# Kernel optimization log

Hardware: AMD Instinct MI355X
Metric: run time of the kernel (lower is better)

Reference implementation:

```python
import jax, jax.numpy as jnp
import numpy as np

HIDDEN_DIM = 4096
NUM_EXPERTS = 64
TOP_K = 2
TEMPERATURE = 1.0
NUM_TOKENS = 16384


def setup_inputs() -> dict:
    key = jax.random.key(0)
    kx, kw = jax.random.split(key)
    x = jax.random.normal(kx, (NUM_TOKENS, HIDDEN_DIM), dtype=jnp.float32)
    # nn.Linear(hidden_dim, num_experts, bias=False): weight shape [num_experts, hidden_dim]
    W = jax.random.normal(kw, (NUM_EXPERTS, HIDDEN_DIM), dtype=jnp.float32) * (1.0 / np.sqrt(HIDDEN_DIM))
    return {"x": x, "W": W}


def reference(x, W):
    # gate linear: [N, H] @ [H, E] -> [N, E]
    logits = jnp.einsum("nh,eh->ne", x, W) / TEMPERATURE
    probs = jax.nn.softmax(logits, axis=-1)

    top_k_probs, top_k_indices = jax.lax.top_k(probs, TOP_K)  # [N, k]
    top_k_weights = top_k_probs / jnp.sum(top_k_probs, axis=-1, keepdims=True)

    # ---- stats (fused histogram instead of per-expert loop) ----
    expert_counts = jnp.zeros((NUM_EXPERTS,), dtype=jnp.float32).at[top_k_indices.ravel()].add(1.0)
    avg_probs = jnp.mean(probs, axis=0)
    entropy = jnp.mean(-jnp.sum(probs * jnp.log(probs + 1e-10), axis=-1))
    sorted_counts = jnp.sort(expert_counts)
    n = NUM_EXPERTS
    index = jnp.arange(1, n + 1, dtype=jnp.float32)
    gini = jnp.sum((2.0 * index - n - 1.0) * sorted_counts) / (n * jnp.sum(sorted_counts) + 1e-10)

    return (top_k_indices, top_k_weights, expert_counts, avg_probs, entropy, gini)
```

## Files before the change

### kernel.cpp

```cpp
#include <hip/hip_runtime.h>
#include <cstdint>
#include <cstddef>

#define NTOK 16384
#define HID  4096
#define NEXP 64
#define MT   128
#define KT   32
#define TPB_A 128

__device__ __forceinline__ void gload_lds16(const float* gp, float* lp) {
  __builtin_amdgcn_global_load_lds(
      (const __attribute__((address_space(1))) void*)gp,
      (__attribute__((address_space(3))) void*)lp,
      16, 0, 0);
}

__global__ __launch_bounds__(TPB_A) void gemm_part_kernel(
    const float* __restrict__ x, const float* __restrict__ W,
    float* __restrict__ part, int KS) {
  const int ntile = NTOK / MT;
  const int tile  = blockIdx.x % ntile;
  const int ks    = blockIdx.x / ntile;
  const int KRANGE = HID / KS;
  const int NKT    = KRANGE / KT;
  const int k0     = ks * KRANGE;
  const int t0     = tile * MT;

  __shared__ float xs[2][MT * KT];
  __shared__ float wsh[2][NEXP * KT];

  const int tid  = threadIdx.x;
  const int lane = tid & 63;
  const int wave = tid >> 6;
  const int tg   = tid >> 3;
  const int eg   = tid & 7;

  float acc[8][8];
#pragma unroll
  for (int i = 0; i < 8; ++i)
#pragma unroll
    for (int j = 0; j < 8; ++j) acc[i][j] = 0.f;

  auto stage = [&](int b, int kt) {
    const int kbase = k0 + kt * KT;
#pragma unroll
    for (int s = 0; s < 8; ++s) {
      int chunk = s * 2 + wave;
      int Lb  = chunk * 1024 + lane * 16;
      int row = Lb >> 7;
      int k4s = (Lb >> 4) & 7;
      int gk4 = k4s ^ (row & 7);
      const float* gp = x + (size_t)(t0 + row) * HID + kbase + gk4 * 4;
      gload_lds16(gp, &xs[b][chunk * 256]);
    }
#pragma unroll
    for (int s = 0; s < 4; ++s) {
      int chunk = s * 2 + wave;
      int Lb  = chunk * 1024 + lane * 16;
      int e   = Lb >> 7;
      int k4s = (Lb >> 4) & 7;
      int gk4 = k4s ^ ((e >> 3) & 7);
      const float* gp = W + (size_t)e * HID + kbase + gk4 * 4;
      gload_lds16(gp, &wsh[b][chunk * 256]);
    }
  };

  auto compute = [&](int b) {
    for (int k4 = 0; k4 < 8; ++k4) {
      float4 xv[8], wv[8];
#pragma unroll
      for (int i = 0; i < 8; ++i) {
        int t = tg + 16 * i;
        xv[i] = *(const float4*)&xs[b][t * 32 + ((k4 ^ (tg & 7)) << 2)];
      }
#pragma unroll
      for (int j = 0; j < 8; ++j) {
        int e = eg * 8 + j;
        wv[j] = *(const float4*)&wsh[b][e * 32 + ((k4 ^ eg) << 2)];
      }
#pragma unroll
      for (int i = 0; i < 8; ++i)
#pragma unroll
        for (int j = 0; j < 8; ++j) {
          acc[i][j] = fmaf(xv[i].x, wv[j].x, acc[i][j]);
          acc[i][j] = fmaf(xv[i].y, wv[j].y, acc[i][j]);
          acc[i][j] = fmaf(xv[i].z, wv[j].z, acc[i][j]);
          acc[i][j] = fmaf(xv[i].w, wv[j].w, acc[i][j]);
        }
    }
  };

  stage(0, 0);
  __syncthreads();
  for (int kt = 0; kt < NKT; ++kt) {
    if (kt + 1 < NKT) stage((kt + 1) & 1, kt + 1);
    compute(kt & 1);
    __syncthreads();
  }

  float* pb = part + ((size_t)ks * NTOK + t0) * NEXP;
#pragma unroll
  for (int i = 0; i < 8; ++i) {
    int t = tg + 16 * i;
    float4 o0 = make_float4(acc[i][0], acc[i][1], acc[i][2], acc[i][3]);
    float4 o1 = make_float4(acc[i][4], acc[i][5], acc[i][6], acc[i][7]);
    *(float4*)&pb[(size_t)t * NEXP + eg * 8]     = o0;
    *(float4*)&pb[(size_t)t * NEXP + eg * 8 + 4] = o1;
  }
}

__global__ __launch_bounds__(256) void router_kernel(
    const float* __restrict__ part, float* __restrict__ out,
    float* __restrict__ gstats, int KS) {
  const int lane  = threadIdx.x & 63;
  const int wave  = threadIdx.x >> 6;
  const int tbase = blockIdx.x * 64 + wave * 16;

  float avg_acc = 0.f, ent_acc = 0.f, cnt_acc = 0.f;

  for (int tt = 0; tt < 16; ++tt) {
    const int t = tbase + tt;
    float l = 0.f;
    for (int s = 0; s < KS; ++s)
      l += part[((size_t)s * NTOK + t) * NEXP + lane];

    float m = l;
#pragma unroll
    for (int off = 32; off; off >>= 1) m = fmaxf(m, __shfl_xor(m, off));
    float p = expf(l - m);
    float d = p;
#pragma unroll
    for (int off = 32; off; off >>= 1) d += __shfl_xor(d, off);
    float prob = p / d;

    avg_acc += prob;
    ent_acc += prob * logf(prob + 1e-10f);

    float v1 = prob; int i1 = lane;
#pragma unroll
    for (int off = 32; off; off >>= 1) {
      float ov = __shfl_xor(v1, off);
      int   oi = __shfl_xor(i1, off);
      if (ov > v1 || (ov == v1 && oi < i1)) { v1 = ov; i1 = oi; }
    }
    float v2 = (lane == i1) ? -1.f : prob; int i2 = lane;
#pragma unroll
    for (int off = 32; off; off >>= 1) {
      float ov = __shfl_xor(v2, off);
      int   oi = __shfl_xor(i2, off);
      if (ov > v2 || (ov == v2 && oi < i2)) { v2 = ov; i2 = oi; }
    }
    cnt_acc += (lane == i1 ? 1.f : 0.f) + (lane == i2 ? 1.f : 0.f);

    if (lane == 0) {
      float wsum = v1 + v2;
      out[2 * t]     = (float)i1;
      out[2 * t + 1] = (float)i2;
      out[2 * NTOK + 2 * t]     = v1 / wsum;
      out[2 * NTOK + 2 * t + 1] = v2 / wsum;
    }
  }

  __shared__ float red[4][NEXP];
  red[wave][lane] = avg_acc;
  __syncthreads();
  if (wave == 0) {
    float s = red[0][lane] + red[1][lane] + red[2][lane] + red[3][lane];
    atomicAdd(&gstats[NEXP + lane], s);
  }
  __syncthreads();
  red[wave][lane] = cnt_acc;
  __syncthreads();
  if (wave == 0) {
    float s = red[0][lane] + red[1][lane] + red[2][lane] + red[3][lane];
    atomicAdd(&gstats[lane], s);
  }
  float e = ent_acc;
#pragma unroll
  for (int off = 32; off; off >>= 1) e += __shfl_xor(e, off);
  __syncthreads();
  if (lane == 0) red[0][wave] = e;
  __syncthreads();
  if (threadIdx.x == 0)
    atomicAdd(&gstats[2 * NEXP], red[0][0] + red[0][1] + red[0][2] + red[0][3]);
}

__global__ void finalize_kernel(const float* __restrict__ gstats,
                                float* __restrict__ out) {
  const int e = threadIdx.x;
  const float c   = gstats[e];
  const float avg = gstats[NEXP + e] * (1.0f / NTOK);

  out[2 * NTOK * 2 + e]        = c;
  out[2 * NTOK * 2 + NEXP + e] = avg;

  __shared__ float cs[NEXP];
  cs[e] = c;
  __syncthreads();

  int rank = 0;
  for (int j = 0; j < NEXP; ++j) {
    float cj = cs[j];
    rank += (cj < c || (cj == c && j < e)) ? 1 : 0;
  }
  float val = (2.0f * (rank + 1) - NEXP - 1) * c;
  float tot = c;
#pragma unroll
  for (int off = 32; off; off >>= 1) {
    val += __shfl_xor(val, off);
    tot += __shfl_xor(tot, off);
  }
  if (e == 0) {
    out[2 * NTOK * 2 + 2 * NEXP]     = -gstats[2 * NEXP] * (1.0f / NTOK);
    out[2 * NTOK * 2 + 2 * NEXP + 1] = val / (NEXP * tot + 1e-10f);
  }
}

extern "C" void kernel_launch(void* const* d_in, const int* in_sizes, int n_in,
                              void* d_out, int out_size, void* d_ws, size_t ws_size,
                              hipStream_t stream) {
  const float* x = (const float*)d_in[0];
  const float* W = (const float*)d_in[1];
  float* out = (float*)d_out;
  float* ws  = (float*)d_ws;

  int KS;
  const size_t slab = (size_t)NTOK * NEXP * 4;
  const size_t stats_bytes = (2 * NEXP + 1) * sizeof(float);
  if      (ws_size >= 8 * slab + stats_bytes) KS = 8;
  else if (ws_size >= 4 * slab + stats_bytes) KS = 4;
  else if (ws_size >= 2 * slab + stats_bytes) KS = 2;
  else                                        KS = 1;

  float* gstats = ws + (size_t)KS * NTOK * NEXP;
  hipMemsetAsync(gstats, 0, stats_bytes, stream);

  gemm_part_kernel<<<dim3((NTOK / MT) * KS), TPB_A, 0, stream>>>(x, W, ws, KS);
  router_kernel<<<dim3(NTOK / 64), 256, 0, stream>>>(ws, out, gstats, KS);
  finalize_kernel<<<dim3(1), 64, 0, stream>>>(gstats, out);
}
```

Baseline: 503.3 us.

## Fuse gate GEMM and routing into one MFMA kernel with split-fp16 precision

Replaces the FP32 SIMT split-K GEMM plus separate router kernel with one fused kernel. It splits x and W into hi/lo fp16 pairs and uses three fp16 MFMA products to approximate fp32 accuracy, then does softmax, top-2, entropy and the stats reductions in-register with LDS atomics. This removes the partial-sum workspace round trip and the FP32 FMA compute bound. In exchange it adds per-element conversion work, direct global loads without LDS staging, and a small accuracy risk from dropping the lo*lo term.

```diff
diff --git a/kernel.cpp b/kernel.cpp
--- a/kernel.cpp
+++ b/kernel.cpp
@@ -5,185 +5,218 @@
 #define NTOK 16384
 #define HID  4096
 #define NEXP 64
-#define MT   128
-#define KT   32
-#define TPB_A 128
-
-__device__ __forceinline__ void gload_lds16(const float* gp, float* lp) {
-  __builtin_amdgcn_global_load_lds(
-      (const __attribute__((address_space(1))) void*)gp,
-      (__attribute__((address_space(3))) void*)lp,
-      16, 0, 0);
-}
-
-__global__ __launch_bounds__(TPB_A) void gemm_part_kernel(
-    const float* __restrict__ x, const float* __restrict__ W,
-    float* __restrict__ part, int KS) {
-  const int ntile = NTOK / MT;
-  const int tile  = blockIdx.x % ntile;
-  const int ks    = blockIdx.x / ntile;
-  const int KRANGE = HID / KS;
-  const int NKT    = KRANGE / KT;
-  const int k0     = ks * KRANGE;
-  const int t0     = tile * MT;
-
-  __shared__ float xs[2][MT * KT];
-  __shared__ float wsh[2][NEXP * KT];
-
-  const int tid  = threadIdx.x;
-  const int lane = tid & 63;
-  const int wave = tid >> 6;
-  const int tg   = tid >> 3;
-  const int eg   = tid & 7;
-
-  float acc[8][8];
-#pragma unroll
-  for (int i = 0; i < 8; ++i)
-#pragma unroll
-    for (int j = 0; j < 8; ++j) acc[i][j] = 0.f;
-
-  auto stage = [&](int b, int kt) {
-    const int kbase = k0 + kt * KT;
-#pragma unroll
-    for (int s = 0; s < 8; ++s) {
-      int chunk = s * 2 + wave;
-      int Lb  = chunk * 1024 + lane * 16;
-      int row = Lb >> 7;
-      int k4s = (Lb >> 4) & 7;
-      int gk4 = k4s ^ (row & 7);
-      const float* gp = x + (size_t)(t0 + row) * HID + kbase + gk4 * 4;
-      gload_lds16(gp, &xs[b][chunk * 256]);
-    }
-#pragma unroll
-    for (int s = 0; s < 4; ++s) {
-      int chunk = s * 2 + wave;
-      int Lb  = chunk * 1024 + lane * 16;
-      int e   = Lb >> 7;
-      int k4s = (Lb >> 4) & 7;
-      int gk4 = k4s ^ ((e >> 3) & 7);
-      const float* gp = W + (size_t)e * HID + kbase + gk4 * 4;
-      gload_lds16(gp, &wsh[b][chunk * 256]);
-    }
-  };
-
-  auto compute = [&](int b) {
-    for (int k4 = 0; k4 < 8; ++k4) {
-      float4 xv[8], wv[8];
-#pragma unroll
-      for (int i = 0; i < 8; ++i) {
-        int t = tg + 16 * i;
-        xv[i] = *(const float4*)&xs[b][t * 32 + ((k4 ^ (tg & 7)) << 2)];
-      }
-#pragma unroll
-      for (int j = 0; j < 8; ++j) {
-        int e = eg * 8 + j;
-        wv[j] = *(const float4*)&wsh[b][e * 32 + ((k4 ^ eg) << 2)];
-      }
-#pragma unroll
-      for (int i = 0; i < 8; ++i)
-#pragma unroll
-        for (int j = 0; j < 8; ++j) {
-          acc[i][j] = fmaf(xv[i].x, wv[j].x, acc[i][j]);
-          acc[i][j] = fmaf(xv[i].y, wv[j].y, acc[i][j]);
-          acc[i][j] = fmaf(xv[i].z, wv[j].z, acc[i][j]);
-          acc[i][j] = fmaf(xv[i].w, wv[j].w, acc[i][j]);
+#define LO_SCALE 2048.0f
+#define LO_INV   (1.0f/2048.0f)
+
+typedef _Float16 half8  __attribute__((ext_vector_type(8)));
+typedef _Float16 half4v __attribute__((ext_vector_type(4)));
+typedef float    f32x4  __attribute__((ext_vector_type(4)));
+
+__global__ __launch_bounds__(256) void wsplit_kernel(
+    const float* __restrict__ W, _Float16* __restrict__ whi,
+    _Float16* __restrict__ wlo) {
+  int i = (blockIdx.x * 256 + threadIdx.x) * 4;
+  float4 w = *(const float4*)(W + i);
+  float f[4] = {w.x, w.y, w.z, w.w};
+  half4v h, l;
+#pragma unroll
+  for (int j = 0; j < 4; ++j) {
+    float hf = __uint_as_float(__float_as_uint(f[j]) & 0xffffe000u);
+    h[j] = (_Float16)hf;
+    l[j] = (_Float16)((f[j] - hf) * LO_SCALE);
+  }
+  *(half4v*)(whi + i) = h;
+  *(half4v*)(wlo + i) = l;
+}
+
+__global__ __launch_bounds__(256, 2) void fused_kernel(
+    const float* __restrict__ x, const _Float16* __restrict__ whi,
+    const _Float16* __restrict__ wlo, float* __restrict__ out,
+    float* __restrict__ gstats) {
+  __shared__ float red[32][NEXP];
+  __shared__ float savg[NEXP];
+  __shared__ float scnt[NEXP];
+  __shared__ float sent;
+
+  const int tid     = threadIdx.x;
+  const int lane    = tid & 63;
+  const int wv      = tid >> 6;
+  const int tokhalf = wv & 1;
+  const int khalf   = wv >> 1;
+  const int row     = lane & 15;
+  const int g       = lane >> 4;
+
+  if (tid < NEXP) { savg[tid] = 0.f; scnt[tid] = 0.f; }
+  if (tid == 0) sent = 0.f;
+
+  const int t0 = blockIdx.x * 32 + tokhalf * 16;
+  const float*    xp  = x   + (size_t)(t0 + row) * HID + khalf * 2048 + g * 8;
+  const _Float16* whp = whi + (size_t)row * HID        + khalf * 2048 + g * 8;
+  const _Float16* wlp = wlo + (size_t)row * HID        + khalf * 2048 + g * 8;
+  const size_t estride = (size_t)16 * HID;
+
+  f32x4 acc[4], crs[4];
+#pragma unroll
+  for (int e = 0; e < 4; ++e) {
+    acc[e] = (f32x4){0.f, 0.f, 0.f, 0.f};
+    crs[e] = (f32x4){0.f, 0.f, 0.f, 0.f};
+  }
+
+#define LDA(KS, P0, P1)                              \
+  P0 = *(const float4*)(xp + (KS) * 32);             \
+  P1 = *(const float4*)(xp + (KS) * 32 + 4);
+
+#define LDB(KS, BH, BL)                                        \
+  _Pragma("unroll")                                            \
+  for (int e = 0; e < 4; ++e) {                                \
+    BH[e] = *(const half8*)(whp + e * estride + (KS) * 32);    \
+    BL[e] = *(const half8*)(wlp + e * estride + (KS) * 32);    \
+  }
+
+#define STEP(P0, P1, BH, BL)                                              \
+  {                                                                       \
+    float ff[8] = {P0.x, P0.y, P0.z, P0.w, P1.x, P1.y, P1.z, P1.w};       \
+    half8 ah, al;                                                         \
+    _Pragma("unroll")                                                     \
+    for (int j = 0; j < 8; ++j) {                                         \
+      float hf = __uint_as_float(__float_as_uint(ff[j]) & 0xffffe000u);   \
+      ah[j] = (_Float16)hf;                                               \
+      al[j] = (_Float16)((ff[j] - hf) * LO_SCALE);                        \
+    }                                                                     \
+    _Pragma("unroll")                                                     \
+    for (int e = 0; e < 4; ++e) {                                         \
+      acc[e] = __builtin_amdgcn_mfma_f32_16x16x32_f16(ah, BH[e], acc[e], 0, 0, 0); \
+      crs[e] = __builtin_amdgcn_mfma_f32_16x16x32_f16(ah, BL[e], crs[e], 0, 0, 0); \
+      crs[e] = __builtin_amdgcn_mfma_f32_16x16x32_f16(al, BH[e], crs[e], 0, 0, 0); \
+    }                                                                     \
+  }
+
+  float4 xa0, xa1, xb0, xb1;
+  half8 bh0[4], bl0[4], bh1[4], bl1[4];
+
+  LDA(0, xa0, xa1)
+  LDB(0, bh0, bl0)
+  for (int ks = 0; ks < 64; ks += 2) {
+    LDA(ks + 1, xb0, xb1)
+    LDB(ks + 1, bh1, bl1)
+    STEP(xa0, xa1, bh0, bl0)
+    if (ks + 2 < 64) {
+      LDA(ks + 2, xa0, xa1)
+      LDB(ks + 2, bh0, bl0)
+    }
+    STEP(xb0, xb1, bh1, bl1)
+  }
+
+  float v[4][4];
+#pragma unroll
+  for (int e = 0; e < 4; ++e)
+#pragma unroll
+    for (int r = 0; r < 4; ++r)
+      v[e][r] = acc[e][r] + crs[e][r] * LO_INV;
+
+  if (khalf == 1) {
+#pragma unroll
+    for (int e = 0; e < 4; ++e)
+#pragma unroll
+      for (int r = 0; r < 4; ++r)
+        red[tokhalf * 16 + g * 4 + r][e * 16 + row] = v[e][r];
+  }
+  __syncthreads();
+
+  if (khalf == 0) {
+#pragma unroll
+    for (int e = 0; e < 4; ++e)
+#pragma unroll
+      for (int r = 0; r < 4; ++r)
+        v[e][r] += red[tokhalf * 16 + g * 4 + r][e * 16 + row];
+
+    float m[4], S[4], PL[4];
+#pragma unroll
+    for (int r = 0; r < 4; ++r) {
+      float mm = fmaxf(fmaxf(v[0][r], v[1][r]), fmaxf(v[2][r], v[3][r]));
+#pragma unroll
+      for (int off = 1; off < 16; off <<= 1) mm = fmaxf(mm, __shfl_xor(mm, off));
+      m[r] = mm;
+    }
+    float p[4][4];
+#pragma unroll
+    for (int e = 0; e < 4; ++e)
+#pragma unroll
+      for (int r = 0; r < 4; ++r)
+        p[e][r] = __expf(v[e][r] - m[r]);
+#pragma unroll
+    for (int r = 0; r < 4; ++r) {
+      float s  = p[0][r] + p[1][r] + p[2][r] + p[3][r];
+      float pl = p[0][r] * v[0][r] + p[1][r] * v[1][r] +
+                 p[2][r] * v[2][r] + p[3][r] * v[3][r];
+#pragma unroll
+      for (int off = 1; off < 16; off <<= 1) {
+        s  += __shfl_xor(s, off);
+        pl += __shfl_xor(pl, off);
+      }
+      S[r] = s; PL[r] = pl;
+    }
+
+    float v1[4], v2[4]; int i1[4], i2[4];
+#pragma unroll
+    for (int r = 0; r < 4; ++r) {
+      float a1 = -3.4e38f, a2 = -3.4e38f; int j1 = 0, j2 = 0;
+#pragma unroll
+      for (int e = 0; e < 4; ++e) {
+        float val = v[e][r]; int idx = e * 16 + row;
+        if (val > a1)      { a2 = a1; j2 = j1; a1 = val; j1 = idx; }
+        else if (val > a2) { a2 = val; j2 = idx; }
+      }
+#pragma unroll
+      for (int off = 1; off < 16; off <<= 1) {
+        float o1 = __shfl_xor(a1, off), o2 = __shfl_xor(a2, off);
+        int  oj1 = __shfl_xor(j1, off), oj2 = __shfl_xor(j2, off);
+        if (o1 > a1 || (o1 == a1 && oj1 < j1)) {
+          if (a1 > o2 || (a1 == o2 && j1 < oj2)) { a2 = a1; j2 = j1; }
+          else                                   { a2 = o2; j2 = oj2; }
+          a1 = o1; j1 = oj1;
+        } else if (o1 > a2 || (o1 == a2 && oj1 < j2)) {
+          a2 = o1; j2 = oj1;
         }
-    }
-  };
-
-  stage(0, 0);
+      }
+      v1[r] = a1; v2[r] = a2; i1[r] = j1; i2[r] = j2;
+    }
+
+    float inv[4] = {1.f / S[0], 1.f / S[1], 1.f / S[2], 1.f / S[3]};
+
+#pragma unroll
+    for (int e = 0; e < 4; ++e) {
+      float s = p[e][0] * inv[0] + p[e][1] * inv[1] +
+                p[e][2] * inv[2] + p[e][3] * inv[3];
+      s += __shfl_xor(s, 16);
+      s += __shfl_xor(s, 32);
+      if (lane < 16) atomicAdd(&savg[e * 16 + row], s);
+    }
+
+    if (row == 0) {
+      float hsum = 0.f;
+#pragma unroll
+      for (int r = 0; r < 4; ++r) {
+        hsum += m[r] + __logf(S[r]) - PL[r] * inv[r];
+        atomicAdd(&scnt[i1[r]], 1.f);
+        atomicAdd(&scnt[i2[r]], 1.f);
+        int t = t0 + g * 4 + r;
+        float e2 = __expf(v2[r] - v1[r]);
+        float w1 = 1.f / (1.f + e2);
+        out[2 * t]     = (float)i1[r];
+        out[2 * t + 1] = (float)i2[r];
+        out[2 * NTOK + 2 * t]     = w1;
+        out[2 * NTOK + 2 * t + 1] = e2 * w1;
+      }
+      atomicAdd(&sent, hsum);
+    }
+  }
   __syncthreads();
-  for (int kt = 0; kt < NKT; ++kt) {
-    if (kt + 1 < NKT) stage((kt + 1) & 1, kt + 1);
-    compute(kt & 1);
-    __syncthreads();
-  }
-
-  float* pb = part + ((size_t)ks * NTOK + t0) * NEXP;
-#pragma unroll
-  for (int i = 0; i < 8; ++i) {
-    int t = tg + 16 * i;
-    float4 o0 = make_float4(acc[i][0], acc[i][1], acc[i][2], acc[i][3]);
-    float4 o1 = make_float4(acc[i][4], acc[i][5], acc[i][6], acc[i][7]);
-    *(float4*)&pb[(size_t)t * NEXP + eg * 8]     = o0;
-    *(float4*)&pb[(size_t)t * NEXP + eg * 8 + 4] = o1;
-  }
-}
-
-__global__ __launch_bounds__(256) void router_kernel(
-    const float* __restrict__ part, float* __restrict__ out,
-    float* __restrict__ gstats, int KS) {
-  const int lane  = threadIdx.x & 63;
-  const int wave  = threadIdx.x >> 6;
-  const int tbase = blockIdx.x * 64 + wave * 16;
-
-  float avg_acc = 0.f, ent_acc = 0.f, cnt_acc = 0.f;
-
-  for (int tt = 0; tt < 16; ++tt) {
-    const int t = tbase + tt;
-    float l = 0.f;
-    for (int s = 0; s < KS; ++s)
-      l += part[((size_t)s * NTOK + t) * NEXP + lane];
-
-    float m = l;
-#pragma unroll
-    for (int off = 32; off; off >>= 1) m = fmaxf(m, __shfl_xor(m, off));
-    float p = expf(l - m);
-    float d = p;
-#pragma unroll
-    for (int off = 32; off; off >>= 1) d += __shfl_xor(d, off);
-    float prob = p / d;
-
-    avg_acc += prob;
-    ent_acc += prob * logf(prob + 1e-10f);
-
-    float v1 = prob; int i1 = lane;
-#pragma unroll
-    for (int off = 32; off; off >>= 1) {
-      float ov = __shfl_xor(v1, off);
-      int   oi = __shfl_xor(i1, off);
-      if (ov > v1 || (ov == v1 && oi < i1)) { v1 = ov; i1 = oi; }
-    }
-    float v2 = (lane == i1) ? -1.f : prob; int i2 = lane;
-#pragma unroll
-    for (int off = 32; off; off >>= 1) {
-      float ov = __shfl_xor(v2, off);
-      int   oi = __shfl_xor(i2, off);
-      if (ov > v2 || (ov == v2 && oi < i2)) { v2 = ov; i2 = oi; }
-    }
-    cnt_acc += (lane == i1 ? 1.f : 0.f) + (lane == i2 ? 1.f : 0.f);
-
-    if (lane == 0) {
-      float wsum = v1 + v2;
-      out[2 * t]     = (float)i1;
-      out[2 * t + 1] = (float)i2;
-      out[2 * NTOK + 2 * t]     = v1 / wsum;
-      out[2 * NTOK + 2 * t + 1] = v2 / wsum;
-    }
-  }
-
-  __shared__ float red[4][NEXP];
-  red[wave][lane] = avg_acc;
-  __syncthreads();
-  if (wave == 0) {
-    float s = red[0][lane] + red[1][lane] + red[2][lane] + red[3][lane];
-    atomicAdd(&gstats[NEXP + lane], s);
-  }
-  __syncthreads();
-  red[wave][lane] = cnt_acc;
-  __syncthreads();
-  if (wave == 0) {
-    float s = red[0][lane] + red[1][lane] + red[2][lane] + red[3][lane];
-    atomicAdd(&gstats[lane], s);
-  }
-  float e = ent_acc;
-#pragma unroll
-  for (int off = 32; off; off >>= 1) e += __shfl_xor(e, off);
-  __syncthreads();
-  if (lane == 0) red[0][wave] = e;
-  __syncthreads();
-  if (threadIdx.x == 0)
-    atomicAdd(&gstats[2 * NEXP], red[0][0] + red[0][1] + red[0][2] + red[0][3]);
+  if (tid < NEXP) {
+    atomicAdd(&gstats[tid],        scnt[tid]);
+    atomicAdd(&gstats[NEXP + tid], savg[tid]);
+  }
+  if (tid == 0) atomicAdd(&gstats[2 * NEXP], sent);
 }
 
 __global__ void finalize_kernel(const float* __restrict__ gstats,
@@ -192,8 +225,8 @@
   const float c   = gstats[e];
   const float avg = gstats[NEXP + e] * (1.0f / NTOK);
 
-  out[2 * NTOK * 2 + e]        = c;
-  out[2 * NTOK * 2 + NEXP + e] = avg;
+  out[4 * NTOK + e]        = c;
+  out[4 * NTOK + NEXP + e] = avg;
 
   __shared__ float cs[NEXP];
   cs[e] = c;
@@ -212,8 +245,8 @@
     tot += __shfl_xor(tot, off);
   }
   if (e == 0) {
-    out[2 * NTOK * 2 + 2 * NEXP]     = -gstats[2 * NEXP] * (1.0f / NTOK);
-    out[2 * NTOK * 2 + 2 * NEXP + 1] = val / (NEXP * tot + 1e-10f);
+    out[4 * NTOK + 2 * NEXP]     = gstats[2 * NEXP] * (1.0f / NTOK);
+    out[4 * NTOK + 2 * NEXP + 1] = val / (NEXP * tot + 1e-10f);
   }
 }
 
@@ -223,20 +256,13 @@
   const float* x = (const float*)d_in[0];
   const float* W = (const float*)d_in[1];
   float* out = (float*)d_out;
-  float* ws  = (float*)d_ws;
-
-  int KS;
-  const size_t slab = (size_t)NTOK * NEXP * 4;
-  const size_t stats_bytes = (2 * NEXP + 1) * sizeof(float);
-  if      (ws_size >= 8 * slab + stats_bytes) KS = 8;
-  else if (ws_size >= 4 * slab + stats_bytes) KS = 4;
-  else if (ws_size >= 2 * slab + stats_bytes) KS = 2;
-  else                                        KS = 1;
-
-  float* gstats = ws + (size_t)KS * NTOK * NEXP;
-  hipMemsetAsync(gstats, 0, stats_bytes, stream);
-
-  gemm_part_kernel<<<dim3((NTOK / MT) * KS), TPB_A, 0, stream>>>(x, W, ws, KS);
-  router_kernel<<<dim3(NTOK / 64), 256, 0, stream>>>(ws, out, gstats, KS);
+
+  _Float16* whi = (_Float16*)d_ws;
+  _Float16* wlo = whi + (size_t)NEXP * HID;
+  float* gstats = (float*)(wlo + (size_t)NEXP * HID);
+
+  hipMemsetAsync(gstats, 0, (2 * NEXP + 1) * sizeof(float), stream);
+  wsplit_kernel<<<dim3((NEXP * HID) / (256 * 4)), 256, 0, stream>>>(W, whi, wlo);
+  fused_kernel<<<dim3(NTOK / 32), 256, 0, stream>>>(x, whi, wlo, out, gstats);
   finalize_kernel<<<dim3(1), 64, 0, stream>>>(gstats, out);
 }
```

After: 460.7 us. -8.5%, faster.
